# Kernel optimization log

Hardware: AMD Instinct MI355X
Metric: run time of the kernel (lower is better)

The kernel has to match this reference:

```python
import jax, jax.numpy as jnp
import numpy as np

B, T, E, HID, V, K = 32, 512, 512, 512, 50257, 12
H = HID // 2          # per-direction LSTM hidden
START, STOP = 10, 11  # tag_to_ix['<START>'], tag_to_ix['<STOP>']
NEG = -10000.0


def setup_inputs() -> dict:
    key = jax.random.key(0)
    ks = jax.random.split(key, 16)
    sentence = jax.random.randint(ks[0], (B, T), 0, V)
    embed = jax.random.normal(ks[1], (V, E), jnp.float32) * 0.1
    # torch LSTM weights, gate order (i, f, g, o); biases fused (b_ih + b_hh)
    w_ih_f = jax.random.normal(ks[2], (4 * H, E), jnp.float32) * 0.05
    w_hh_f = jax.random.normal(ks[3], (4 * H, H), jnp.float32) * 0.05
    b_f = jax.random.normal(ks[4], (4 * H,), jnp.float32) * 0.05
    w_ih_b = jax.random.normal(ks[5], (4 * H, E), jnp.float32) * 0.05
    w_hh_b = jax.random.normal(ks[6], (4 * H, H), jnp.float32) * 0.05
    b_b = jax.random.normal(ks[7], (4 * H,), jnp.float32) * 0.05
    # init_hidden(): random initial states, [2 directions, B, H]
    h0 = jax.random.normal(ks[8], (2, B, H), jnp.float32)
    c0 = jax.random.normal(ks[9], (2, B, H), jnp.float32)
    W_out = jax.random.normal(ks[10], (K, HID), jnp.float32) * 0.05
    b_out = jax.random.normal(ks[11], (K,), jnp.float32) * 0.05
    transitions = jax.random.normal(ks[12], (K, K), jnp.float32)
    transitions = transitions.at[START, :].set(NEG).at[:, STOP].set(NEG)
    return dict(sentence=sentence, embed=embed,
                w_ih_f=w_ih_f, w_hh_f=w_hh_f, b_f=b_f,
                w_ih_b=w_ih_b, w_hh_b=w_hh_b, b_b=b_b,
                h0=h0, c0=c0, W_out=W_out, b_out=b_out,
                transitions=transitions)


def _lstm_dir(x, w_ih, w_hh, b, h0, c0, reverse):
    # x: [B, T, E] -> hidden sequence [B, T, H]
    xg = jnp.einsum('bte,ge->btg', x, w_ih) + b  # [B, T, 4H] input pre-activations

    def step(carry, xt):
        h, c = carry
        g = xt + h @ w_hh.T
        i, f, gg, o = jnp.split(g, 4, axis=-1)
        c = jax.nn.sigmoid(f) * c + jax.nn.sigmoid(i) * jnp.tanh(gg)
        h = jax.nn.sigmoid(o) * jnp.tanh(c)
        return (h, c), h

    _, ys = jax.lax.scan(step, (h0, c0), jnp.swapaxes(xg, 0, 1), reverse=reverse)
    return jnp.swapaxes(ys, 0, 1)


def reference(sentence, embed, w_ih_f, w_hh_f, b_f, w_ih_b, w_hh_b, b_b,
              h0, c0, W_out, b_out, transitions):
    # _get_lstm_features
    x = embed[sentence]  # [B, T, E]
    hf = _lstm_dir(x, w_ih_f, w_hh_f, b_f, h0[0], c0[0], False)
    hb = _lstm_dir(x, w_ih_b, w_hh_b, b_b, h0[1], c0[1], True)
    feats = jnp.concatenate([hf, hb], axis=-1) @ W_out.T + b_out  # [B, T, K]

    # _viterbi_decode: fused per-timestep max/argmax recurrence
    init = jnp.full((B, K), NEG, jnp.float32).at[:, START].set(0.0)

    def vstep(fv, feat_t):
        # scores[b, next, prev] = fv[b, prev] + transitions[next, prev]
        scores = fv[:, None, :] + transitions[None, :, :]
        bptr = jnp.argmax(scores, axis=2)            # [B, K]
        fv_new = jnp.max(scores, axis=2) + feat_t     # emit score added after max
        return fv_new, bptr

    fv, bptrs = jax.lax.scan(vstep, init, jnp.swapaxes(feats, 0, 1))  # bptrs [T, B, K]
    terminal = fv + transitions[STOP]                 # [B, K]
    best = jnp.argmax(terminal, axis=1)               # [B]
    # faithful to original: terminal_var[:, best_tag_id] -> [B, B]
    path_score = jnp.take(terminal, best, axis=1)

    def back(tag, bp):
        prev = jnp.take_along_axis(bp, tag[:, None], axis=1)[:, 0]
        return prev, prev

    _, ys = jax.lax.scan(back, best, bptrs, reverse=True)  # ys[t] = tag at position t-1
    # path positions 0..T-1 are (ys[1:], best); ys[0] is START (dropped by [:,1:])
    best_path = jnp.concatenate([ys[1:], best[None, :]], axis=0).T  # [B, T]
    return path_score, best_path
```

## Files before the change

### kernel.cpp

```cpp
#include <hip/hip_runtime.h>
#include <hip/hip_bf16.h>


typedef __attribute__((ext_vector_type(8))) __bf16 bf16x8;
typedef __attribute__((ext_vector_type(4))) float  f32x4;
typedef __attribute__((ext_vector_type(4))) unsigned int u32x4;

#define MFMA16(a, b, c) __builtin_amdgcn_mfma_f32_16x16x32_bf16((a), (b), (c), 0, 0, 0)

__device__ __forceinline__ float sigm(float x) { return 1.0f / (1.0f + __expf(-x)); }
__device__ __forceinline__ float tanh_f(float x) {
  x = fminf(fmaxf(x, -15.0f), 15.0f);
  float e = __expf(2.0f * x);
  return (e - 1.0f) / (e + 1.0f);
}

__device__ __forceinline__ void split8(const float* v, bf16x8& hi, bf16x8& lo) {
#pragma unroll
  for (int j = 0; j < 8; j++) {
    __bf16 h = (__bf16)v[j];
    hi[j] = h;
    lo[j] = (__bf16)(v[j] - (float)h);
  }
}

__global__ __launch_bounds__(256) void xg_gemm(
    const int* __restrict__ sent, const float* __restrict__ embed,
    const float* __restrict__ wih_f, const float* __restrict__ wih_b,
    const float* __restrict__ bias_f, const float* __restrict__ bias_b,
    float* __restrict__ xg)
{
  __shared__ __bf16 Ah[128][40], Al[128][40];
  __shared__ __bf16 Bh[128][40], Bl[128][40];
  __shared__ int toks[128];
  const int tid = threadIdx.x;
  const int m0 = blockIdx.x * 128, n0 = blockIdx.y * 128;
  if (tid < 128) toks[tid] = sent[m0 + tid];
  const int wave = tid >> 6, lane = tid & 63, q = lane >> 4, c = lane & 15;
  const int wy = wave >> 1, wx = wave & 1;
  f32x4 acc[4][4];
  for (int mt = 0; mt < 4; mt++)
    for (int nt = 0; nt < 4; nt++)
      acc[mt][nt] = f32x4{0.0f, 0.0f, 0.0f, 0.0f};
  __syncthreads();

  for (int k0 = 0; k0 < 512; k0 += 32) {
#pragma unroll
    for (int i = 0; i < 2; i++) {
      int ch = tid + (i << 8);
      int r = ch >> 2, kc = ch & 3;
      float tmp[8];
      const float* asrc = embed + (size_t)toks[r] * 512 + k0 + kc * 8;
#pragma unroll
      for (int j = 0; j < 8; j++) tmp[j] = asrc[j];
      bf16x8 hi, lo;
      split8(tmp, hi, lo);
      *(bf16x8*)&Ah[r][kc * 8] = hi;
      *(bf16x8*)&Al[r][kc * 8] = lo;
      int n = n0 + r;
      const float* wsrc = (n < 1024) ? (wih_f + (size_t)n * 512)
                                     : (wih_b + (size_t)(n - 1024) * 512);
#pragma unroll
      for (int j = 0; j < 8; j++) tmp[j] = wsrc[k0 + kc * 8 + j];
      split8(tmp, hi, lo);
      *(bf16x8*)&Bh[r][kc * 8] = hi;
      *(bf16x8*)&Bl[r][kc * 8] = lo;
    }
    __syncthreads();
    bf16x8 ah[4], al[4], bh[4], bl[4];
#pragma unroll
    for (int t4 = 0; t4 < 4; t4++) {
      int ar = wy * 64 + t4 * 16 + c, br = wx * 64 + t4 * 16 + c;
      ah[t4] = *(const bf16x8*)&Ah[ar][q * 8];
      al[t4] = *(const bf16x8*)&Al[ar][q * 8];
      bh[t4] = *(const bf16x8*)&Bh[br][q * 8];
      bl[t4] = *(const bf16x8*)&Bl[br][q * 8];
    }
#pragma unroll
    for (int mt = 0; mt < 4; mt++)
#pragma unroll
      for (int nt = 0; nt < 4; nt++) {
        acc[mt][nt] = MFMA16(ah[mt], bh[nt], acc[mt][nt]);
        acc[mt][nt] = MFMA16(al[mt], bh[nt], acc[mt][nt]);
        acc[mt][nt] = MFMA16(ah[mt], bl[nt], acc[mt][nt]);
      }
    __syncthreads();
  }

#pragma unroll
  for (int nt = 0; nt < 4; nt++) {
    int n = n0 + wx * 64 + nt * 16 + c;
    float bval = (n < 1024) ? bias_f[n] : bias_b[n - 1024];
#pragma unroll
    for (int mt = 0; mt < 4; mt++) {
      int mbase = m0 + wy * 64 + mt * 16 + q * 4;
#pragma unroll
      for (int reg = 0; reg < 4; reg++)
        xg[(size_t)(mbase + reg) * 2048 + n] = acc[mt][nt][reg] + bval;
    }
  }
}

__global__ __launch_bounds__(256, 1) void lstm_rec(
    const float* __restrict__ xg,
    const float* __restrict__ whh_f, const float* __restrict__ whh_b,
    const float* __restrict__ h0, const float* __restrict__ c0,
    float* __restrict__ h_seq,
    unsigned int* __restrict__ hx,
    int* __restrict__ flags)
{
  const int blk = blockIdx.x;
  const int d = blk >> 2, hs = blk & 3;
  const int tid = threadIdx.x;
  const int wave = tid >> 6, lane = tid & 63, q = lane >> 4, c = lane & 15;
  const float* __restrict__ whh = d ? whh_b : whh_f;

  __shared__ __bf16 hfrag[2][2][16][512];

  bf16x8 wfh[4][8], wfl[4][8];
#pragma unroll
  for (int g = 0; g < 4; g++) {
    int row = g * 256 + hs * 64 + wave * 16 + c;
    const float* wr = whh + (size_t)row * 256;
#pragma unroll
    for (int ks = 0; ks < 8; ks++) {
      float tmp[8];
#pragma unroll
      for (int j = 0; j < 8; j++) tmp[j] = wr[ks * 32 + q * 8 + j];
      split8(tmp, wfh[g][ks], wfl[g][ks]);
    }
  }
  const int ug = hs * 64 + wave * 16 + c;
  float cst[2][4];
#pragma unroll
  for (int mt = 0; mt < 2; mt++)
#pragma unroll
    for (int reg = 0; reg < 4; reg++)
      cst[mt][reg] = c0[d * 8192 + (mt * 16 + q * 4 + reg) * 256 + ug];

  const int sb = tid >> 3;
  const int kc4 = (tid & 7) * 4;

  int fid_c[4], pos_c[4];
#pragma unroll
  for (int i = 0; i < 4; i++) {
    int kc = kc4 + i;
    fid_c[i] = ((sb >> 4) << 3) + (kc >> 2);
    pos_c[i] = ((((kc & 3) << 4) + (sb & 15)) ^ (fid_c[i] & 7));
  }

  const unsigned long long* hb64p[2];
  hb64p[0] = (const unsigned long long*)(hx + ((size_t)((d * 2 + 0) * 32 + sb)) * 256 + kc4 * 8);
  hb64p[1] = (const unsigned long long*)(hx + ((size_t)((d * 2 + 1) * 32 + sb)) * 256 + kc4 * 8);
  const int hwbase0 = (d * 2 + 0) * 32 * 256 + ug;
  const int hwbase1 = (d * 2 + 1) * 32 * 256 + ug;
  int bof[2][4];
#pragma unroll
  for (int mt = 0; mt < 2; mt++)
#pragma unroll
    for (int reg = 0; reg < 4; reg++)
      bof[mt][reg] = (mt * 16 + q * 4 + reg) * 256;

  int fro = (d * 512) * 16 + (lane & 15);
  int fwo = (d * 512) * 16 + hs * 4 + wave;

  const int t0 = d ? 511 : 0;
  const int tdelt = d ? -2048 : 2048;
  const int sdelt = d ? -512 : 512;

  int xgo[2][4], hso[2][4];
#pragma unroll
  for (int mt = 0; mt < 2; mt++)
#pragma unroll
    for (int reg = 0; reg < 4; reg++) {
      int b = mt * 16 + q * 4 + reg;
      xgo[mt][reg] = (b * 512 + t0) * 2048 + (d << 10) + ug;
      hso[mt][reg] = (b * 512 + t0) * 512 + (d << 8) + ug;
    }

  float xvA[2][4][4], xvB[2][4][4];
#pragma unroll
  for (int mt = 0; mt < 2; mt++)
#pragma unroll
    for (int reg = 0; reg < 4; reg++)
#pragma unroll
      for (int g = 0; g < 4; g++)
        xvA[mt][g][reg] = xg[xgo[mt][reg] + (g << 8)];

#define LSTM_STEP(S_, P_, XC_, XN_)                                           \
  {                                                                           \
    if ((S_) == 0) {                                                          \
      _Pragma("unroll")                                                       \
      for (int i = 0; i < 4; i++) {                                           \
        int kc = kc4 + i;                                                     \
        float tmp[8];                                                         \
        const float* src = h0 + d * 8192 + sb * 256 + kc * 8;                 \
        _Pragma("unroll")                                                     \
        for (int j = 0; j < 8; j++) tmp[j] = src[j];                          \
        bf16x8 vhi, vlo;                                                      \
        split8(tmp, vhi, vlo);                                                \
        *(bf16x8*)&hfrag[0][0][fid_c[i]][pos_c[i] * 8] = vhi;                 \
        *(bf16x8*)&hfrag[0][1][fid_c[i]][pos_c[i] * 8] = vlo;                 \
      }                                                                       \
    } else {                                                                  \
      int fv = __hip_atomic_load(flags + fro, __ATOMIC_RELAXED,               \
                                 __HIP_MEMORY_SCOPE_AGENT);                   \
      while (!__all(fv == (S_))) {                                            \
        __builtin_amdgcn_s_sleep(1);                                          \
        fv = __hip_atomic_load(flags + fro, __ATOMIC_RELAXED,                 \
                               __HIP_MEMORY_SCOPE_AGENT);                     \
      }                                                                       \
      fro += 16;                                                              \
      unsigned long long v64[16];                                             \
      _Pragma("unroll")                                                       \
      for (int i = 0; i < 16; i++)                                            \
        v64[i] = __hip_atomic_load(hb64p[P_] + i, __ATOMIC_RELAXED,           \
                                   __HIP_MEMORY_SCOPE_AGENT);                 \
      _Pragma("unroll")                                                       \
      for (int i = 0; i < 4; i++) {                                           \
        u32x4 vh, vl;                                                         \
        _Pragma("unroll")                                                     \
        for (int k = 0; k < 4; k++) {                                         \
          unsigned int lo32 = (unsigned int)v64[i * 4 + k];                   \
          unsigned int hi32 = (unsigned int)(v64[i * 4 + k] >> 32);           \
          vh[k] = __builtin_amdgcn_perm(hi32, lo32, 0x07060302u);             \
          vl[k] = __builtin_amdgcn_perm(hi32, lo32, 0x05040100u);             \
        }                                                                     \
        *(u32x4*)&hfrag[P_][0][fid_c[i]][pos_c[i] * 8] = vh;                  \
        *(u32x4*)&hfrag[P_][1][fid_c[i]][pos_c[i] * 8] = vl;                  \
      }                                                                       \
    }                                                                         \
    f32x4 acc[2][4];                                                          \
    _Pragma("unroll")                                                         \
    for (int mt = 0; mt < 2; mt++)                                            \
      _Pragma("unroll")                                                       \
      for (int g = 0; g < 4; g++)                                             \
        _Pragma("unroll")                                                     \
        for (int reg = 0; reg < 4; reg++)                                     \
          acc[mt][g][reg] = XC_[mt][g][reg];                                  \
    __syncthreads();                                                          \
    _Pragma("unroll")                                                         \
    for (int ks = 0; ks < 8; ks++) {                                          \
      int pos = (lane ^ ks) * 8;                                              \
      bf16x8 ahi0 = *(const bf16x8*)&hfrag[P_][0][ks][pos];                   \
      bf16x8 ahi1 = *(const bf16x8*)&hfrag[P_][0][8 + ks][pos];               \
      bf16x8 alo0 = *(const bf16x8*)&hfrag[P_][1][ks][pos];                   \
      bf16x8 alo1 = *(const bf16x8*)&hfrag[P_][1][8 + ks][pos];               \
      _Pragma("unroll")                                                       \
      for (int g = 0; g < 4; g++) {                                           \
        acc[0][g] = MFMA16(ahi0, wfh[g][ks], acc[0][g]);                      \
        acc[1][g] = MFMA16(ahi1, wfh[g][ks], acc[1][g]);                      \
        acc[0][g] = MFMA16(alo0, wfh[g][ks], acc[0][g]);                      \
        acc[1][g] = MFMA16(alo1, wfh[g][ks], acc[1][g]);                      \
        acc[0][g] = MFMA16(ahi0, wfl[g][ks], acc[0][g]);                      \
        acc[1][g] = MFMA16(ahi1, wfl[g][ks], acc[1][g]);                      \
      }                                                                       \
    }                                                                         \
    float hv[2][4];                                                           \
    _Pragma("unroll")                                                         \
    for (int mt = 0; mt < 2; mt++)                                            \
      _Pragma("unroll")                                                       \
      for (int reg = 0; reg < 4; reg++) {                                     \
        float iv = sigm(acc[mt][0][reg]);                                     \
        float fg = sigm(acc[mt][1][reg]);                                     \
        float gv = tanh_f(acc[mt][2][reg]);                                   \
        float ov = sigm(acc[mt][3][reg]);                                     \
        float cn = fg * cst[mt][reg] + iv * gv;                               \
        cst[mt][reg] = cn;                                                    \
        float hn = ov * tanh_f(cn);                                           \
        hv[mt][reg] = hn;                                                     \
        __bf16 hhi = (__bf16)hn;                                              \
        __bf16 hlo = (__bf16)(hn - (float)hhi);                               \
        unsigned int pack =                                                   \
            ((unsigned int)__builtin_bit_cast(unsigned short, hhi) << 16) |   \
            (unsigned int)__builtin_bit_cast(unsigned short, hlo);            \
        __hip_atomic_store(hx + ((P_) ? hwbase0 : hwbase1) + bof[mt][reg],    \
                           pack, __ATOMIC_RELAXED, __HIP_MEMORY_SCOPE_AGENT); \
      }                                                                       \
    asm volatile("s_waitcnt vmcnt(0)" ::: "memory");                          \
    if (lane == 0)                                                            \
      __hip_atomic_store(flags + fwo, (S_) + 1, __ATOMIC_RELAXED,             \
                         __HIP_MEMORY_SCOPE_AGENT);                           \
    fwo += 16;                                                                \
    _Pragma("unroll")                                                         \
    for (int mt = 0; mt < 2; mt++)                                            \
      _Pragma("unroll")                                                       \
      for (int reg = 0; reg < 4; reg++)                                       \
        h_seq[hso[mt][reg]] = hv[mt][reg];                                    \
    if ((S_) < 511) {                                                         \
      _Pragma("unroll")                                                       \
      for (int mt = 0; mt < 2; mt++)                                          \
        _Pragma("unroll")                                                     \
        for (int reg = 0; reg < 4; reg++) {                                   \
          xgo[mt][reg] += tdelt;                                              \
          hso[mt][reg] += sdelt;                                              \
        }                                                                     \
      _Pragma("unroll")                                                       \
      for (int mt = 0; mt < 2; mt++)                                          \
        _Pragma("unroll")                                                     \
        for (int reg = 0; reg < 4; reg++)                                     \
          _Pragma("unroll")                                                   \
          for (int g = 0; g < 4; g++)                                         \
            XN_[mt][g][reg] = xg[xgo[mt][reg] + (g << 8)];                    \
    }                                                                         \
  }

  for (int s = 0; s < 512; s += 2) {
    LSTM_STEP(s,     0, xvA, xvB);
    LSTM_STEP(s + 1, 1, xvB, xvA);
  }
#undef LSTM_STEP
}

__global__ __launch_bounds__(256) void feats_k(
    const float* __restrict__ h_seq, const float* __restrict__ W_out,
    const float* __restrict__ b_out, float* __restrict__ feats)
{
  int m = blockIdx.x * 4 + (threadIdx.x >> 6);
  int lane = threadIdx.x & 63;
  const float4* hp = (const float4*)(h_seq + (size_t)m * 512 + lane * 8);
  float4 a = hp[0], b2 = hp[1];
  float h[8] = {a.x, a.y, a.z, a.w, b2.x, b2.y, b2.z, b2.w};
#pragma unroll
  for (int k = 0; k < 12; k++) {
    const float4* wp = (const float4*)(W_out + k * 512 + lane * 8);
    float4 w0 = wp[0], w1 = wp[1];
    float w[8] = {w0.x, w0.y, w0.z, w0.w, w1.x, w1.y, w1.z, w1.w};
    float p = 0.0f;
#pragma unroll
    for (int j = 0; j < 8; j++) p += h[j] * w[j];
#pragma unroll
    for (int off = 32; off > 0; off >>= 1) p += __shfl_xor(p, off);
    if (lane == 0) feats[(size_t)m * 12 + k] = p + b_out[k];
  }
}

__global__ __launch_bounds__(64) void viterbi_k(
    const float* __restrict__ feats, const float* __restrict__ trans,
    float* __restrict__ terminal, int* __restrict__ best,
    float* __restrict__ out_path)
{
  const int b = blockIdx.x;
  const int lane = threadIdx.x;
  __shared__ unsigned char bp[512][12];
  float trow[12];
#pragma unroll
  for (int pv = 0; pv < 12; pv++)
    trow[pv] = (lane < 12) ? trans[lane * 12 + pv] : -10000.0f;
  float fv = (lane == 10) ? 0.0f : -10000.0f;
  for (int t = 0; t < 512; t++) {
    float bestv = -3.4e38f;
    int arg = 0;
#pragma unroll
    for (int pv = 0; pv < 12; pv++) {
      float sc = __shfl(fv, pv) + trow[pv];
      if (sc > bestv) { bestv = sc; arg = pv; }
    }
    float ft = (lane < 12) ? feats[(size_t)(b * 512 + t) * 12 + lane] : 0.0f;
    if (lane < 12) {
      bp[t][lane] = (unsigned char)arg;
      fv = bestv + ft;
    }
  }
  float term = fv + ((lane < 12) ? trans[11 * 12 + lane] : 0.0f);
  if (lane < 12) terminal[b * 12 + lane] = term;
  float v = (lane < 12) ? term : -3.4e38f;
  int idx = lane;
#pragma unroll
  for (int off = 8; off > 0; off >>= 1) {
    float ov = __shfl_down(v, off);
    int oi = __shfl_down(idx, off);
    if (ov > v || (ov == v && oi < idx)) { v = ov; idx = oi; }
  }
  int bidx = __shfl(idx, 0);
  __syncthreads();
  if (lane == 0) {
    best[b] = bidx;
    int tag = bidx;
    out_path[b * 512 + 511] = (float)bidx;
    for (int t = 511; t >= 1; t--) {
      tag = bp[t][tag];
      out_path[b * 512 + t - 1] = (float)tag;
    }
  }
}

__global__ __launch_bounds__(256) void pscore_k(
    const float* __restrict__ terminal, const int* __restrict__ best,
    float* __restrict__ out)
{
  int idx = blockIdx.x * 256 + threadIdx.x;
  if (idx < 1024) {
    int i = idx >> 5, j = idx & 31;
    out[idx] = terminal[i * 12 + best[j]];
  }
}

extern "C" void kernel_launch(void* const* d_in, const int* in_sizes, int n_in,
                              void* d_out, int out_size, void* d_ws, size_t ws_size,
                              hipStream_t stream)
{
  const int*   sent  = (const int*)d_in[0];
  const float* embed = (const float*)d_in[1];
  const float* wih_f = (const float*)d_in[2];
  const float* whh_f = (const float*)d_in[3];
  const float* b_f   = (const float*)d_in[4];
  const float* wih_b = (const float*)d_in[5];
  const float* whh_b = (const float*)d_in[6];
  const float* b_b   = (const float*)d_in[7];
  const float* h0    = (const float*)d_in[8];
  const float* c0    = (const float*)d_in[9];
  const float* W_out = (const float*)d_in[10];
  const float* b_out = (const float*)d_in[11];
  const float* trans = (const float*)d_in[12];

  char* ws = (char*)d_ws;
  float*        xg    = (float*)(ws);
  float*        h_seq = (float*)(ws + 134217728);
  float*        feats = (float*)(ws + 167772160);
  unsigned int* hx    = (unsigned int*)(ws + 168558592);
  int*          flags = (int*)(ws + 168689664);
  float*        term  = (float*)(ws + 168755200);
  int*          best  = (int*)(ws + 168756736);

  float* outp = (float*)d_out;

  hipMemsetAsync(flags, 0, 2 * 512 * 16 * sizeof(int), stream);
  xg_gemm<<<dim3(128, 16), 256, 0, stream>>>(sent, embed, wih_f, wih_b, b_f, b_b, xg);
  lstm_rec<<<8, 256, 0, stream>>>(xg, whh_f, whh_b, h0, c0, h_seq, hx, flags);
  feats_k<<<4096, 256, 0, stream>>>(h_seq, W_out, b_out, feats);
  viterbi_k<<<32, 64, 0, stream>>>(feats, trans, term, best, outp + 1024);
  pscore_k<<<4, 256, 0, stream>>>(term, best, outp);
}
```

Measured before the change: 3.856 ms.

## Embed step tags in hidden-state words to replace separate flag synchronization

The cross-block LSTM recurrence exchange now stores each packed bf16 hi/lo hidden value together with a step tag in a single 64-bit atomic word. Consumers poll the data words directly until every tag matches, so the separate flag array, the vmcnt(0) drain and the flag store/poll round trip are gone. This is meant to shorten the per-timestep inter-block handoff latency on the serial critical path. In exchange it doubles the exchange buffer size and makes readers spin on many more words. It also reuses workspace that overlaps the feats region, which is safe only because feats is written later.

```diff
diff --git a/kernel.cpp b/kernel.cpp
--- a/kernel.cpp
+++ b/kernel.cpp
@@ -106,8 +106,7 @@
     const float* __restrict__ whh_f, const float* __restrict__ whh_b,
     const float* __restrict__ h0, const float* __restrict__ c0,
     float* __restrict__ h_seq,
-    unsigned int* __restrict__ hx,
-    int* __restrict__ flags)
+    unsigned long long* __restrict__ hx)
 {
   const int blk = blockIdx.x;
   const int d = blk >> 2, hs = blk & 3;
@@ -150,8 +149,8 @@
   }
 
   const unsigned long long* hb64p[2];
-  hb64p[0] = (const unsigned long long*)(hx + ((size_t)((d * 2 + 0) * 32 + sb)) * 256 + kc4 * 8);
-  hb64p[1] = (const unsigned long long*)(hx + ((size_t)((d * 2 + 1) * 32 + sb)) * 256 + kc4 * 8);
+  hb64p[0] = hx + ((size_t)((d * 2 + 0) * 32 + sb)) * 256 + kc4 * 8;
+  hb64p[1] = hx + ((size_t)((d * 2 + 1) * 32 + sb)) * 256 + kc4 * 8;
   const int hwbase0 = (d * 2 + 0) * 32 * 256 + ug;
   const int hwbase1 = (d * 2 + 1) * 32 * 256 + ug;
   int bof[2][4];
@@ -160,9 +159,6 @@
 #pragma unroll
     for (int reg = 0; reg < 4; reg++)
       bof[mt][reg] = (mt * 16 + q * 4 + reg) * 256;
-
-  int fro = (d * 512) * 16 + (lane & 15);
-  int fwo = (d * 512) * 16 + hs * 4 + wave;
 
   const int t0 = d ? 511 : 0;
   const int tdelt = d ? -2048 : 2048;
@@ -203,31 +199,42 @@
         *(bf16x8*)&hfrag[0][1][fid_c[i]][pos_c[i] * 8] = vlo;                 \
       }                                                                       \
     } else {                                                                  \
-      int fv = __hip_atomic_load(flags + fro, __ATOMIC_RELAXED,               \
-                                 __HIP_MEMORY_SCOPE_AGENT);                   \
-      while (!__all(fv == (S_))) {                                            \
-        __builtin_amdgcn_s_sleep(1);                                          \
-        fv = __hip_atomic_load(flags + fro, __ATOMIC_RELAXED,                 \
-                               __HIP_MEMORY_SCOPE_AGENT);                     \
-      }                                                                       \
-      fro += 16;                                                              \
-      unsigned long long v64[16];                                             \
-      _Pragma("unroll")                                                       \
-      for (int i = 0; i < 16; i++)                                            \
-        v64[i] = __hip_atomic_load(hb64p[P_] + i, __ATOMIC_RELAXED,           \
+      const unsigned int tagw = (unsigned int)(S_);                           \
+      const unsigned long long* hb = hb64p[P_];                               \
+      _Pragma("unroll")                                                       \
+      for (int r2 = 0; r2 < 2; r2++) {                                        \
+        unsigned long long v[16];                                             \
+        _Pragma("unroll")                                                     \
+        for (int i = 0; i < 16; i++)                                          \
+          v[i] = __hip_atomic_load(hb + r2 * 16 + i, __ATOMIC_RELAXED,        \
                                    __HIP_MEMORY_SCOPE_AGENT);                 \
-      _Pragma("unroll")                                                       \
-      for (int i = 0; i < 4; i++) {                                           \
-        u32x4 vh, vl;                                                         \
-        _Pragma("unroll")                                                     \
-        for (int k = 0; k < 4; k++) {                                         \
-          unsigned int lo32 = (unsigned int)v64[i * 4 + k];                   \
-          unsigned int hi32 = (unsigned int)(v64[i * 4 + k] >> 32);           \
-          vh[k] = __builtin_amdgcn_perm(hi32, lo32, 0x07060302u);             \
-          vl[k] = __builtin_amdgcn_perm(hi32, lo32, 0x05040100u);             \
+        while (true) {                                                        \
+          unsigned int bad = 0;                                               \
+          _Pragma("unroll")                                                   \
+          for (int i = 0; i < 16; i++)                                        \
+            bad |= ((unsigned int)(v[i] >> 32)) ^ tagw;                       \
+          if (__all(bad == 0)) break;                                         \
+          __builtin_amdgcn_s_sleep(1);                                        \
+          _Pragma("unroll")                                                   \
+          for (int i = 0; i < 16; i++)                                        \
+            if (((unsigned int)(v[i] >> 32)) != tagw)                         \
+              v[i] = __hip_atomic_load(hb + r2 * 16 + i, __ATOMIC_RELAXED,    \
+                                       __HIP_MEMORY_SCOPE_AGENT);             \
         }                                                                     \
-        *(u32x4*)&hfrag[P_][0][fid_c[i]][pos_c[i] * 8] = vh;                  \
-        *(u32x4*)&hfrag[P_][1][fid_c[i]][pos_c[i] * 8] = vl;                  \
+        _Pragma("unroll")                                                     \
+        for (int i2 = 0; i2 < 2; i2++) {                                      \
+          int ci = r2 * 2 + i2;                                               \
+          u32x4 vh, vl;                                                       \
+          _Pragma("unroll")                                                   \
+          for (int k = 0; k < 4; k++) {                                       \
+            unsigned int a0 = (unsigned int)v[i2 * 8 + 2 * k];                \
+            unsigned int a1 = (unsigned int)v[i2 * 8 + 2 * k + 1];            \
+            vh[k] = __builtin_amdgcn_perm(a1, a0, 0x07060302u);               \
+            vl[k] = __builtin_amdgcn_perm(a1, a0, 0x05040100u);               \
+          }                                                                   \
+          *(u32x4*)&hfrag[P_][0][fid_c[ci]][pos_c[ci] * 8] = vh;              \
+          *(u32x4*)&hfrag[P_][1][fid_c[ci]][pos_c[ci] * 8] = vl;              \
+        }                                                                     \
       }                                                                       \
     }                                                                         \
     f32x4 acc[2][4];                                                          \
@@ -256,6 +263,7 @@
         acc[1][g] = MFMA16(ahi1, wfl[g][ks], acc[1][g]);                      \
       }                                                                       \
     }                                                                         \
+    const unsigned long long tagst = ((unsigned long long)((S_) + 1)) << 32;  \
     float hv[2][4];                                                           \
     _Pragma("unroll")                                                         \
     for (int mt = 0; mt < 2; mt++)                                            \
@@ -275,13 +283,9 @@
             ((unsigned int)__builtin_bit_cast(unsigned short, hhi) << 16) |   \
             (unsigned int)__builtin_bit_cast(unsigned short, hlo);            \
         __hip_atomic_store(hx + ((P_) ? hwbase0 : hwbase1) + bof[mt][reg],    \
-                           pack, __ATOMIC_RELAXED, __HIP_MEMORY_SCOPE_AGENT); \
+                           tagst | (unsigned long long)pack,                  \
+                           __ATOMIC_RELAXED, __HIP_MEMORY_SCOPE_AGENT);       \
       }                                                                       \
-    asm volatile("s_waitcnt vmcnt(0)" ::: "memory");                          \
-    if (lane == 0)                                                            \
-      __hip_atomic_store(flags + fwo, (S_) + 1, __ATOMIC_RELAXED,             \
-                         __HIP_MEMORY_SCOPE_AGENT);                           \
-    fwo += 16;                                                                \
     _Pragma("unroll")                                                         \
     for (int mt = 0; mt < 2; mt++)                                            \
       _Pragma("unroll")                                                       \
@@ -415,19 +419,18 @@
   const float* trans = (const float*)d_in[12];
 
   char* ws = (char*)d_ws;
-  float*        xg    = (float*)(ws);
-  float*        h_seq = (float*)(ws + 134217728);
-  float*        feats = (float*)(ws + 167772160);
-  unsigned int* hx    = (unsigned int*)(ws + 168558592);
-  int*          flags = (int*)(ws + 168689664);
-  float*        term  = (float*)(ws + 168755200);
-  int*          best  = (int*)(ws + 168756736);
+  float*              xg    = (float*)(ws);
+  float*              h_seq = (float*)(ws + 134217728);
+  float*              feats = (float*)(ws + 167772160);
+  unsigned long long* hx    = (unsigned long long*)(ws + 167772160);
+  float*              term  = (float*)(ws + 168693760);
+  int*                best  = (int*)(ws + 168695296);
 
   float* outp = (float*)d_out;
 
-  hipMemsetAsync(flags, 0, 2 * 512 * 16 * sizeof(int), stream);
+  hipMemsetAsync(hx, 0, 2 * 2 * 32 * 256 * sizeof(unsigned long long), stream);
   xg_gemm<<<dim3(128, 16), 256, 0, stream>>>(sent, embed, wih_f, wih_b, b_f, b_b, xg);
-  lstm_rec<<<8, 256, 0, stream>>>(xg, whh_f, whh_b, h0, c0, h_seq, hx, flags);
+  lstm_rec<<<8, 256, 0, stream>>>(xg, whh_f, whh_b, h0, c0, h_seq, hx);
   feats_k<<<4096, 256, 0, stream>>>(h_seq, W_out, b_out, feats);
   viterbi_k<<<32, 64, 0, stream>>>(feats, trans, term, best, outp + 1024);
   pscore_k<<<4, 256, 0, stream>>>(term, best, outp);
```

Result: slower. 5.299 ms (+37.4%).
